# Optimization experiments

Hardware: AMD Instinct MI355X
Metric: run time of the kernel (lower is better)

The kernel has to match this reference:

```python
import jax, jax.numpy as jnp
import numpy as np

B = 65536
KC = 64   # n_coarse
KF = 64   # n_fine (n_fine_depth = 0)
HID = 32
NEAR, FAR = 2.0, 6.0


def setup_inputs() -> dict:
    key = jax.random.key(0)
    ks = jax.random.split(key, 8)
    origins = jax.random.normal(ks[0], (B, 3), jnp.float32) * 0.1
    dirs = jax.random.normal(ks[1], (B, 3), jnp.float32)
    dirs = dirs / jnp.linalg.norm(dirs, axis=-1, keepdims=True)
    near = jnp.full((B, 1), NEAR, jnp.float32)
    far = jnp.full((B, 1), FAR, jnp.float32)
    rays = jnp.concatenate([origins, dirs, near, far], axis=-1)  # (B, 8)
    u_coarse = jax.random.uniform(ks[2], (B, KC), jnp.float32)
    u_fine = jax.random.uniform(ks[3], (B, KF), jnp.float32)
    u_jitter = jax.random.uniform(ks[4], (B, KF), jnp.float32)
    W1 = jax.random.normal(ks[5], (3, HID), jnp.float32) * 0.5
    b1 = jnp.zeros((HID,), jnp.float32)
    W2 = jax.random.normal(ks[6], (HID, 4), jnp.float32) * 0.5
    b2 = jnp.zeros((4,), jnp.float32)
    return {"rays": rays, "u_coarse": u_coarse, "u_fine": u_fine,
            "u_jitter": u_jitter, "W1": W1, "b1": b1, "W2": W2, "b2": b2}


def _mlp(points, W1, b1, W2, b2):
    # points: (B, K, 3) -> rgb (B, K, 3) in [0,1], sigma (B, K)
    h = jax.nn.relu(jnp.einsum("bkd,dh->bkh", points, W1) + b1)
    o = jnp.einsum("bkh,hc->bkc", h, W2) + b2
    return jax.nn.sigmoid(o[..., :3]), o[..., 3]


def _composite(rays, z_samp, W1, b1, W2, b2):
    # deltas between consecutive samples; last delta up to `far`
    deltas = jnp.concatenate(
        [z_samp[:, 1:] - z_samp[:, :-1], rays[:, -1:] - z_samp[:, -1:]], axis=-1)  # (B, K)
    points = rays[:, None, :3] + z_samp[..., None] * rays[:, None, 3:6]  # (B, K, 3)
    rgbs, sigmas = _mlp(points, W1, b1, W2, b2)
    alphas = 1.0 - jnp.exp(-deltas * jax.nn.relu(sigmas))  # (B, K)
    alphas_shifted = jnp.concatenate(
        [jnp.ones_like(alphas[:, :1]), 1.0 - alphas + 1e-10], axis=-1)
    T = jnp.cumprod(alphas_shifted, axis=-1)  # (B, K+1)
    weights = alphas * T[:, :-1]  # (B, K)
    rgb_final = jnp.sum(weights[..., None] * rgbs, axis=1)  # (B, 3)
    depth_final = jnp.sum(weights * z_samp, axis=1)  # (B,)
    return weights, rgb_final, depth_final


def _sample_coarse(rays, u_coarse):
    near, far = rays[:, -2:-1], rays[:, -1:]
    step = 1.0 / KC
    z_steps = jnp.linspace(0.0, 1.0 - step, KC, dtype=jnp.float32)[None, :] + u_coarse * step
    return near * (1.0 - z_steps) + far * z_steps  # (B, KC), lindisp=False


def _sample_fine(rays, weights, u_fine, u_jitter):
    # inverse-CDF importance sampling; weights are detached in the original
    w = jax.lax.stop_gradient(weights) + 1e-5
    pdf = w / jnp.sum(w, axis=-1, keepdims=True)
    cdf = jnp.cumsum(pdf, axis=-1)
    cdf = jnp.concatenate([jnp.zeros_like(cdf[:, :1]), cdf], axis=-1)  # (B, KC+1)
    inds = jax.vmap(lambda c, u: jnp.searchsorted(c, u, side="right"))(cdf, u_fine)
    inds = jnp.maximum(inds.astype(jnp.float32) - 1.0, 0.0)
    z_steps = (inds + u_jitter) / KC
    near, far = rays[:, -2:-1], rays[:, -1:]
    return near * (1.0 - z_steps) + far * z_steps  # (B, KF)


def reference(rays, u_coarse, u_fine, u_jitter, W1, b1, W2, b2):
    z_coarse = _sample_coarse(rays, u_coarse)
    weights_c, rgb_c, depth_c = _composite(rays, z_coarse, W1, b1, W2, b2)
    z_fine = _sample_fine(rays, weights_c, u_fine, u_jitter)
    z_comb = jnp.sort(jnp.concatenate([z_coarse, z_fine], axis=-1), axis=-1)  # (B, KC+KF)
    weights_f, rgb_f, depth_f = _composite(rays, z_comb, W1, b1, W2, b2)
    return jnp.concatenate(
        [rgb_f, depth_f[:, None], rgb_c, depth_c[:, None]], axis=-1)  # (B, 8)
```

## Files before the change

### kernel.cpp

```cpp
#include <hip/hip_runtime.h>
#include <math.h>


typedef float f32x2 __attribute__((ext_vector_type(2)));
typedef _Float16 f16x2v __attribute__((ext_vector_type(2)));
typedef _Float16 f16x4v __attribute__((ext_vector_type(4)));

__device__ __forceinline__ float fast_rcp(float x) { return __builtin_amdgcn_rcpf(x); }
__device__ __forceinline__ float fsigmoid(float x) { return fast_rcp(1.0f + __expf(-x)); }

__device__ __forceinline__ f32x2 splat_lo(f32x2 v) { return __builtin_shufflevector(v, v, 0, 0); }
__device__ __forceinline__ f32x2 splat_hi(f32x2 v) { return __builtin_shufflevector(v, v, 1, 1); }

__device__ __forceinline__ void wave_fence() {
    asm volatile("" ::: "memory");
    __builtin_amdgcn_wave_barrier();
}

template <int CTRL, int RMASK>
__device__ __forceinline__ float dpp_f(float x, float oldv) {
    return __int_as_float(__builtin_amdgcn_update_dpp(
        __float_as_int(oldv), __float_as_int(x), CTRL, RMASK, 0xf, false));
}
template <int CTRL, int RMASK>
__device__ __forceinline__ int dpp_i(int x, int oldv) {
    return __builtin_amdgcn_update_dpp(oldv, x, CTRL, RMASK, 0xf, false);
}
template <int OFF>
__device__ __forceinline__ float swz_f(float x) {
    return __int_as_float(__builtin_amdgcn_ds_swizzle(__float_as_int(x), OFF));
}

__device__ __forceinline__ float scan_mul(float x) {
    x *= dpp_f<0x111, 0xf>(x, 1.0f);
    x *= dpp_f<0x112, 0xf>(x, 1.0f);
    x *= dpp_f<0x114, 0xf>(x, 1.0f);
    x *= dpp_f<0x118, 0xf>(x, 1.0f);
    x *= dpp_f<0x142, 0xa>(x, 1.0f);
    x *= dpp_f<0x143, 0xc>(x, 1.0f);
    return x;
}
__device__ __forceinline__ float scan_add(float x) {
    x += dpp_f<0x111, 0xf>(x, 0.0f);
    x += dpp_f<0x112, 0xf>(x, 0.0f);
    x += dpp_f<0x114, 0xf>(x, 0.0f);
    x += dpp_f<0x118, 0xf>(x, 0.0f);
    x += dpp_f<0x142, 0xa>(x, 0.0f);
    x += dpp_f<0x143, 0xc>(x, 0.0f);
    return x;
}
__device__ __forceinline__ int scan_add_i(int x) {
    x += dpp_i<0x111, 0xf>(x, 0);
    x += dpp_i<0x112, 0xf>(x, 0);
    x += dpp_i<0x114, 0xf>(x, 0);
    x += dpp_i<0x118, 0xf>(x, 0);
    x += dpp_i<0x142, 0xa>(x, 0);
    x += dpp_i<0x143, 0xc>(x, 0);
    return x;
}

__device__ __forceinline__ float quad_reduce4(float v0, float v1, float v2, float v3, int lane) {
    const bool b0 = (lane & 1) != 0;
    const float w01 = b0 ? v0 : v1, k01 = b0 ? v1 : v0;
    const float x01 = k01 + dpp_f<0xB1, 0xf>(w01, w01);
    const float w23 = b0 ? v2 : v3, k23 = b0 ? v3 : v2;
    const float x23 = k23 + dpp_f<0xB1, 0xf>(w23, w23);
    const bool b1 = (lane & 2) != 0;
    const float w = b1 ? x01 : x23, k = b1 ? x23 : x01;
    float x = k + dpp_f<0x4E, 0xf>(w, w);
    x += dpp_f<0x124, 0xf>(x, x);
    x += dpp_f<0x128, 0xf>(x, x);
    x += swz_f<0x401F>(x);
    x += __shfl_xor(x, 32);
    return x;
}

__global__ __launch_bounds__(256) void nerf_render(
    const float* __restrict__ rays,
    const float* __restrict__ u_coarse,
    const float* __restrict__ u_fine,
    const float* __restrict__ u_jitter,
    const float* __restrict__ W1,
    const float* __restrict__ b1,
    const float* __restrict__ W2,
    const float* __restrict__ b2,
    float* __restrict__ out)
{
    __shared__ f32x2  w2S[64];
    __shared__ float  acS[4][64];
    __shared__ float  zM[4][128];
    __shared__ f16x2v rgM[4][128];
    __shared__ f16x2v bsM[4][128];

    const int lane = threadIdx.x & 63;
    const int wv   = threadIdx.x >> 6;
    const int ray  = (blockIdx.x << 2) + wv;

    const float* rp = rays + ray * 8;
    const float ox = rp[0], oy = rp[1], oz = rp[2];
    const float ddx = rp[3], ddy = rp[4], ddz = rp[5];
    const float nearv = rp[6], farv = rp[7];

    if (threadIdx.x < 64) w2S[threadIdx.x] = reinterpret_cast<const f32x2*>(W2)[threadIdx.x];

    {
        const int j = lane & 31;
        const float w0 = W1[j], w1 = W1[32 + j], w2 = W1[64 + j];
        const bool isA = lane < 32;
        const float px = isA ? ox : ddx;
        const float py = isA ? oy : ddy;
        const float pz = isA ? oz : ddz;
        const float bb = isA ? b1[j] : 0.0f;
        acS[wv][lane] = fmaf(px, w0, fmaf(py, w1, fmaf(pz, w2, bb)));
    }
    __syncthreads();

    const float* aw = &acS[wv][0];
    const float* cw = &acS[wv][32];

    auto mlp = [&](float z, float& rr, float& gg, float& bb_, float& sg) {
        const f32x2 zz = {z, z};
        const f32x2 zero2 = {0.0f, 0.0f};
        f32x2 acc01 = *reinterpret_cast<const f32x2*>(b2);
        f32x2 acc23 = *reinterpret_cast<const f32x2*>(b2 + 2);
#pragma unroll
        for (int j = 0; j < 32; j += 4) {
            const f32x2 a01 = *reinterpret_cast<const f32x2*>(aw + j);
            const f32x2 a23 = *reinterpret_cast<const f32x2*>(aw + j + 2);
            const f32x2 c01 = *reinterpret_cast<const f32x2*>(cw + j);
            const f32x2 c23 = *reinterpret_cast<const f32x2*>(cw + j + 2);
            f32x2 h01 = __builtin_elementwise_fma(zz, c01, a01);
            f32x2 h23 = __builtin_elementwise_fma(zz, c23, a23);
            h01 = __builtin_elementwise_max(h01, zero2);
            h23 = __builtin_elementwise_max(h23, zero2);
            {
                const f32x2 wA = w2S[(j + 0) * 2], wB = w2S[(j + 0) * 2 + 1];
                const f32x2 hs = splat_lo(h01);
                acc01 = __builtin_elementwise_fma(hs, wA, acc01);
                acc23 = __builtin_elementwise_fma(hs, wB, acc23);
            }
            {
                const f32x2 wA = w2S[(j + 1) * 2], wB = w2S[(j + 1) * 2 + 1];
                const f32x2 hs = splat_hi(h01);
                acc01 = __builtin_elementwise_fma(hs, wA, acc01);
                acc23 = __builtin_elementwise_fma(hs, wB, acc23);
            }
            {
                const f32x2 wA = w2S[(j + 2) * 2], wB = w2S[(j + 2) * 2 + 1];
                const f32x2 hs = splat_lo(h23);
                acc01 = __builtin_elementwise_fma(hs, wA, acc01);
                acc23 = __builtin_elementwise_fma(hs, wB, acc23);
            }
            {
                const f32x2 wA = w2S[(j + 3) * 2], wB = w2S[(j + 3) * 2 + 1];
                const f32x2 hs = splat_hi(h23);
                acc01 = __builtin_elementwise_fma(hs, wA, acc01);
                acc23 = __builtin_elementwise_fma(hs, wB, acc23);
            }
        }
        rr = fsigmoid(acc01.x); gg = fsigmoid(acc01.y);
        bb_ = fsigmoid(acc23.x); sg = acc23.y;
    };

    const float uc = u_coarse[ray * 64 + lane];
    const float zsc = (float)lane * 0.015625f + uc * 0.015625f;
    const float zc = nearv * (1.0f - zsc) + farv * zsc;

    const float zcn = dpp_f<0x130, 0xf>(zc, zc);
    const float deltac = (lane == 63) ? (farv - zc) : (zcn - zc);

    float cr_, cg_, cb_, csig;
    mlp(zc, cr_, cg_, cb_, csig);
    const float ec = __expf(-deltac * fmaxf(csig, 0.0f));
    const float alphac = 1.0f - ec;
    const float sc = ec + 1e-10f;

    const float pincl = scan_mul(sc);
    const float Tc = dpp_f<0x138, 0xf>(pincl, 1.0f);
    const float wc = alphac * Tc;

    const float coarseTot = quad_reduce4(wc * cr_, wc * cg_, wc * cb_, wc * zc, lane);

    const float wp = wc + 1e-5f;
    const float cdf = scan_add(wp);
    const float tot = __int_as_float(__builtin_amdgcn_readlane(__float_as_int(cdf), 63));

    const float uf = u_fine[ray * 64 + lane] * tot;
    int cnt = 0;
#pragma unroll
    for (int step = 32; step >= 1; step >>= 1) {
        const float v = __shfl(cdf, cnt + step - 1);
        if (v <= uf) cnt += step;
    }
    const float uj = u_jitter[ray * 64 + lane];
    float key = (float)cnt + uj;

#pragma unroll
    for (int k = 2; k <= 64; k <<= 1) {
#pragma unroll
        for (int j = k >> 1; j > 0; j >>= 1) {
            float v;
            if (j == 1)       v = dpp_f<0xB1, 0xf>(key, key);
            else if (j == 2)  v = dpp_f<0x4E, 0xf>(key, key);
            else if (j == 4)  v = swz_f<0x101F>(key);
            else if (j == 8)  v = swz_f<0x201F>(key);
            else if (j == 16) v = swz_f<0x401F>(key);
            else              v = __shfl_xor(key, 32);
            const bool keepMin = (((lane & j) == 0) == ((lane & k) == 0));
            key = keepMin ? fminf(key, v) : fmaxf(key, v);
        }
    }

    int cnti = (int)key; cnti = cnti > 63 ? 63 : cnti;
    const float ujr = key - (float)cnti;
    const float ucv = __shfl(uc, cnti);
    const int g = cnti + ((ucv <= ujr) ? 1 : 0);
    const int pos_f = lane + g;

    unsigned int* hist = reinterpret_cast<unsigned int*>(&zM[wv][0]);
    hist[lane] = 0u;
    wave_fence();
    atomicAdd(&hist[g], 1u);
    wave_fence();
    const int cfv = scan_add_i((int)hist[lane]);
    const int pos_c = lane + cfv;
    wave_fence();

    const float zsf = key * 0.015625f;
    const float zf = nearv * (1.0f - zsf) + farv * zsf;
    float fr_, fg_, fb_, fsig;
    mlp(zf, fr_, fg_, fb_, fsig);

    {
        zM[wv][pos_c] = zc;
        zM[wv][pos_f] = zf;
        f16x2v t;
        t.x = (_Float16)cr_;  t.y = (_Float16)cg_;  rgM[wv][pos_c] = t;
        t.x = (_Float16)fr_;  t.y = (_Float16)fg_;  rgM[wv][pos_f] = t;
        t.x = (_Float16)cb_;  t.y = (_Float16)csig; bsM[wv][pos_c] = t;
        t.x = (_Float16)fb_;  t.y = (_Float16)fsig; bsM[wv][pos_f] = t;
    }
    wave_fence();

    const float2 zz2 = *reinterpret_cast<const float2*>(&zM[wv][2 * lane]);
    const float z0 = zz2.x, z1 = zz2.y;
    const float z2n = zM[wv][(2 * lane + 2) & 127];
    const f16x4v rg4 = *reinterpret_cast<const f16x4v*>(&rgM[wv][2 * lane]);
    const f16x4v bs4 = *reinterpret_cast<const f16x4v*>(&bsM[wv][2 * lane]);
    const float r0 = (float)rg4.x, g0 = (float)rg4.y;
    const float r1 = (float)rg4.z, g1 = (float)rg4.w;
    const float b0 = (float)bs4.x, s0 = (float)bs4.y;
    const float b1v = (float)bs4.z, s1 = (float)bs4.w;

    const float d0 = z1 - z0;
    const float d1 = (lane == 63) ? (farv - z1) : (z2n - z1);

    const float e0 = __expf(-d0 * fmaxf(s0, 0.0f));
    const float e1 = __expf(-d1 * fmaxf(s1, 0.0f));
    const float al0 = 1.0f - e0;
    const float al1 = 1.0f - e1;
    const float t0 = e0 + 1e-10f;
    const float t1 = e1 + 1e-10f;

    const float ppincl = scan_mul(t0 * t1);
    const float Te = dpp_f<0x138, 0xf>(ppincl, 1.0f);
    const float w0 = al0 * Te;
    const float w1 = al1 * (Te * t0);

    const float fineTot = quad_reduce4(fmaf(w0, r0, w1 * r1), fmaf(w0, g0, w1 * g1),
                                       fmaf(w0, b0, w1 * b1v), fmaf(w0, z0, w1 * z1), lane);

    if (lane < 8) {
        out[ray * 8 + lane] = (lane < 4) ? fineTot : coarseTot;
    }
}

extern "C" void kernel_launch(void* const* d_in, const int* in_sizes, int n_in,
                              void* d_out, int out_size, void* d_ws, size_t ws_size,
                              hipStream_t stream) {
    const float* rays     = (const float*)d_in[0];
    const float* u_coarse = (const float*)d_in[1];
    const float* u_fine   = (const float*)d_in[2];
    const float* u_jitter = (const float*)d_in[3];
    const float* W1       = (const float*)d_in[4];
    const float* b1       = (const float*)d_in[5];
    const float* W2       = (const float*)d_in[6];
    const float* b2       = (const float*)d_in[7];
    float* out = (float*)d_out;

    const int B = in_sizes[0] / 8;
    dim3 grid(B / 4), block(256);
    hipLaunchKernelGGL(nerf_render, grid, block, 0, stream,
                       rays, u_coarse, u_fine, u_jitter, W1, b1, W2, b2, out);
}
```

Before: 75.14 us.

## Drop block barrier, read W2 uniformly, replace histogram atomics with shuffle binary search

Removes the shared-memory W2 copy and reads W2 directly through uniform (scalar-cacheable) global loads, which lets the block-wide __syncthreads become a wave-local fence. The LDS histogram with atomics and integer scan that computed coarse-sample merge positions is replaced by a shuffle-based binary search over the sorted fine bucket indices. The next-z load from LDS is replaced by a DPP lane shift. These cut LDS traffic, atomics and synchronisation, at the cost of six dependent shuffles and possible global-load latency in the MLP loop.

```diff
diff --git a/kernel.cpp b/kernel.cpp
--- a/kernel.cpp
+++ b/kernel.cpp
@@ -21,10 +21,6 @@
 __device__ __forceinline__ float dpp_f(float x, float oldv) {
     return __int_as_float(__builtin_amdgcn_update_dpp(
         __float_as_int(oldv), __float_as_int(x), CTRL, RMASK, 0xf, false));
-}
-template <int CTRL, int RMASK>
-__device__ __forceinline__ int dpp_i(int x, int oldv) {
-    return __builtin_amdgcn_update_dpp(oldv, x, CTRL, RMASK, 0xf, false);
 }
 template <int OFF>
 __device__ __forceinline__ float swz_f(float x) {
@@ -47,15 +43,6 @@
     x += dpp_f<0x118, 0xf>(x, 0.0f);
     x += dpp_f<0x142, 0xa>(x, 0.0f);
     x += dpp_f<0x143, 0xc>(x, 0.0f);
-    return x;
-}
-__device__ __forceinline__ int scan_add_i(int x) {
-    x += dpp_i<0x111, 0xf>(x, 0);
-    x += dpp_i<0x112, 0xf>(x, 0);
-    x += dpp_i<0x114, 0xf>(x, 0);
-    x += dpp_i<0x118, 0xf>(x, 0);
-    x += dpp_i<0x142, 0xa>(x, 0);
-    x += dpp_i<0x143, 0xc>(x, 0);
     return x;
 }
 
@@ -86,7 +73,6 @@
     const float* __restrict__ b2,
     float* __restrict__ out)
 {
-    __shared__ f32x2  w2S[64];
     __shared__ float  acS[4][64];
     __shared__ float  zM[4][128];
     __shared__ f16x2v rgM[4][128];
@@ -100,8 +86,6 @@
     const float ox = rp[0], oy = rp[1], oz = rp[2];
     const float ddx = rp[3], ddy = rp[4], ddz = rp[5];
     const float nearv = rp[6], farv = rp[7];
-
-    if (threadIdx.x < 64) w2S[threadIdx.x] = reinterpret_cast<const f32x2*>(W2)[threadIdx.x];
 
     {
         const int j = lane & 31;
@@ -113,7 +97,7 @@
         const float bb = isA ? b1[j] : 0.0f;
         acS[wv][lane] = fmaf(px, w0, fmaf(py, w1, fmaf(pz, w2, bb)));
     }
-    __syncthreads();
+    wave_fence();
 
     const float* aw = &acS[wv][0];
     const float* cw = &acS[wv][32];
@@ -134,25 +118,29 @@
             h01 = __builtin_elementwise_max(h01, zero2);
             h23 = __builtin_elementwise_max(h23, zero2);
             {
-                const f32x2 wA = w2S[(j + 0) * 2], wB = w2S[(j + 0) * 2 + 1];
+                const f32x2 wA = *reinterpret_cast<const f32x2*>(W2 + (j + 0) * 4);
+                const f32x2 wB = *reinterpret_cast<const f32x2*>(W2 + (j + 0) * 4 + 2);
                 const f32x2 hs = splat_lo(h01);
                 acc01 = __builtin_elementwise_fma(hs, wA, acc01);
                 acc23 = __builtin_elementwise_fma(hs, wB, acc23);
             }
             {
-                const f32x2 wA = w2S[(j + 1) * 2], wB = w2S[(j + 1) * 2 + 1];
+                const f32x2 wA = *reinterpret_cast<const f32x2*>(W2 + (j + 1) * 4);
+                const f32x2 wB = *reinterpret_cast<const f32x2*>(W2 + (j + 1) * 4 + 2);
                 const f32x2 hs = splat_hi(h01);
                 acc01 = __builtin_elementwise_fma(hs, wA, acc01);
                 acc23 = __builtin_elementwise_fma(hs, wB, acc23);
             }
             {
-                const f32x2 wA = w2S[(j + 2) * 2], wB = w2S[(j + 2) * 2 + 1];
+                const f32x2 wA = *reinterpret_cast<const f32x2*>(W2 + (j + 2) * 4);
+                const f32x2 wB = *reinterpret_cast<const f32x2*>(W2 + (j + 2) * 4 + 2);
                 const f32x2 hs = splat_lo(h23);
                 acc01 = __builtin_elementwise_fma(hs, wA, acc01);
                 acc23 = __builtin_elementwise_fma(hs, wB, acc23);
             }
             {
-                const f32x2 wA = w2S[(j + 3) * 2], wB = w2S[(j + 3) * 2 + 1];
+                const f32x2 wA = *reinterpret_cast<const f32x2*>(W2 + (j + 3) * 4);
+                const f32x2 wB = *reinterpret_cast<const f32x2*>(W2 + (j + 3) * 4 + 2);
                 const f32x2 hs = splat_hi(h23);
                 acc01 = __builtin_elementwise_fma(hs, wA, acc01);
                 acc23 = __builtin_elementwise_fma(hs, wB, acc23);
@@ -217,14 +205,15 @@
     const int g = cnti + ((ucv <= ujr) ? 1 : 0);
     const int pos_f = lane + g;
 
-    unsigned int* hist = reinterpret_cast<unsigned int*>(&zM[wv][0]);
-    hist[lane] = 0u;
-    wave_fence();
-    atomicAdd(&hist[g], 1u);
-    wave_fence();
-    const int cfv = scan_add_i((int)hist[lane]);
+    int cfv = 0;
+#pragma unroll
+    for (int step = 32; step >= 1; step >>= 1) {
+        const int v = __shfl(g, cfv + step - 1);
+        if (v <= lane) cfv += step;
+    }
+    const int g63 = __builtin_amdgcn_readlane(g, 63);
+    if (cfv == 63 && g63 <= lane) cfv = 64;
     const int pos_c = lane + cfv;
-    wave_fence();
 
     const float zsf = key * 0.015625f;
     const float zf = nearv * (1.0f - zsf) + farv * zsf;
@@ -244,7 +233,7 @@
 
     const float2 zz2 = *reinterpret_cast<const float2*>(&zM[wv][2 * lane]);
     const float z0 = zz2.x, z1 = zz2.y;
-    const float z2n = zM[wv][(2 * lane + 2) & 127];
+    const float z2n = dpp_f<0x130, 0xf>(z0, z0);
     const f16x4v rg4 = *reinterpret_cast<const f16x4v*>(&rgM[wv][2 * lane]);
     const f16x4v bs4 = *reinterpret_cast<const f16x4v*>(&bsM[wv][2 * lane]);
     const float r0 = (float)rg4.x, g0 = (float)rg4.y;
```

New measurement: 93.48 us. 1.24x slower.
